# Performance work log

Measured on AMD Instinct MI355X. Metric: run time of the kernel, lower is better.

The kernel has to match this reference:

```python
import jax, jax.numpy as jnp
import numpy as np

B, L, D, H, DFF = 8, 1024, 256, 8, 2048
DH = D // H


def setup_inputs() -> dict:
    key = jax.random.key(0)
    ks = jax.random.split(key, 12)

    def w(k, shape):
        return jax.random.normal(k, shape, dtype=jnp.float32) * 0.02

    # continuous padding: first `length` tokens valid, rest padded (mask True = pad)
    lengths = jax.random.randint(ks[0], (B,), L // 4, L + 1)
    mask = jnp.arange(L)[None, :] >= lengths[:, None]

    return {
        "src": jax.random.normal(ks[1], (B, L, D), dtype=jnp.float32),
        "src_key_padding_mask": mask,
        "in_proj_w": w(ks[2], (3 * D, D)),
        "in_proj_b": w(ks[3], (3 * D,)),
        "out_w": w(ks[4], (D, D)),
        "out_b": w(ks[5], (D,)),
        "proj_w": w(ks[6], (D, D)),
        "proj_b": w(ks[7], (D,)),
        "ff1_w": w(ks[8], (DFF, D)),
        "ff1_b": w(ks[9], (DFF,)),
        "ff2_w": w(ks[10], (D, DFF)),
        "ff2_b": w(ks[11], (D,)),
    }


def reference(src, src_key_padding_mask, in_proj_w, in_proj_b, out_w, out_b,
              proj_w, proj_b, ff1_w, ff1_b, ff2_w, ff2_b):
    mask = src_key_padding_mask  # [B, L], True = padding
    neg_inf = jnp.float32(-jnp.inf)

    # --- make_attn_mask (vectorized, continuous padding) ---
    s = (~mask).sum(axis=1).astype(jnp.float32)              # [B] valid lengths
    idx = jnp.arange(L, dtype=jnp.float32)
    dist = jnp.abs(idx[:, None] - idx[None, :])              # [L, L]
    valid_tok = idx[None, :] < s[:, None]                    # [B, L]
    pair_ok = valid_tok[:, :, None] & valid_tok[:, None, :]  # [B, L, L]
    bias = jnp.where(pair_ok, (s[:, None, None] - dist[None]) / s[:, None, None], neg_inf)
    # rows that are entirely -inf (padded query rows) are zeroed, like masked_fill
    row_pad = ~valid_tok                                     # [B, L]
    bias = jnp.where(row_pad[:, :, None], 0.0, bias)
    # key_padding_mask is merged additively (as in nn.MultiheadAttention)
    add_mask = bias + jnp.where(mask[:, None, :], neg_inf, 0.0)  # [B, L, L]

    # --- multi-head self-attention ---
    qkv = src @ in_proj_w.T + in_proj_b                      # [B, L, 3D]
    q, k, v = jnp.split(qkv, 3, axis=-1)

    def heads(t):
        return t.reshape(B, L, H, DH).transpose(0, 2, 1, 3)  # [B, H, L, DH]

    q, k, v = heads(q), heads(k), heads(v)
    scale = 1.0 / jnp.sqrt(jnp.float32(DH))
    scores = jnp.einsum('bhqd,bhkd->bhqk', q, k) * scale + add_mask[:, None]
    attn = jax.nn.softmax(scores, axis=-1)
    ctx = jnp.einsum('bhqk,bhkd->bhqd', attn, v)
    ctx = ctx.transpose(0, 2, 1, 3).reshape(B, L, D)
    h_attn = ctx @ out_w.T + out_b

    # --- residual proj + FFN (no layernorm, no dropout) ---
    h = src + (h_attn @ proj_w.T + proj_b)
    ff = jax.nn.gelu(h @ ff1_w.T + ff1_b, approximate=False) @ ff2_w.T + ff2_b
    h = h + ff

    # zero out padded rows (masked_fill with all_neg_inf)
    h = jnp.where(row_pad[:, :, None], 0.0, h)
    return h
```

## Files before the change

### kernel.cpp

```cpp
#include <hip/hip_runtime.h>
#include <hip/hip_bf16.h>


#define BB   8
#define LL   1024
#define DD   256
#define HHN  8
#define DHH  32
#define DFFN 2048

typedef __attribute__((ext_vector_type(8))) __bf16 bf16x8;
typedef __attribute__((ext_vector_type(4))) float f32x4;

__device__ inline void gload16(const void* g, void* l) {
  __builtin_amdgcn_global_load_lds(
      (const __attribute__((address_space(1))) void*)g,
      (__attribute__((address_space(3))) void*)l, 16, 0, 0);
}

__device__ inline bf16x8 cvt8(const float4 a, const float4 b) {
  bf16x8 o;
  o[0] = (__bf16)a.x; o[1] = (__bf16)a.y; o[2] = (__bf16)a.z; o[3] = (__bf16)a.w;
  o[4] = (__bf16)b.x; o[5] = (__bf16)b.y; o[6] = (__bf16)b.z; o[7] = (__bf16)b.w;
  return o;
}

#define NCVT2 (DFFN * DD)
#define NCVT3 (DD * DFFN)
#define NB_CVT ((NCVT2 + NCVT3) / 2048)

__global__ __launch_bounds__(256) void preamble_kernel(
    const unsigned char* __restrict__ mb, const float* __restrict__ ff1_w,
    const float* __restrict__ ff2_w, const float* __restrict__ proj_w,
    const float* __restrict__ out_w, const float* __restrict__ proj_b,
    const float* __restrict__ out_b, __hip_bfloat16* __restrict__ wff1_bf,
    __hip_bfloat16* __restrict__ wff2_bf, __hip_bfloat16* __restrict__ wc_bf,
    float* __restrict__ bc, int* __restrict__ lens) {
  const int bid = blockIdx.x;
  const int tid = threadIdx.x;
  __shared__ float red[256];
  __shared__ int cnt[BB];
  __shared__ int flag3f, flagNA;

  if (bid < NB_CVT) {
    int i = bid * 2048 + tid * 8;
    const float* s;
    __hip_bfloat16* d;
    if (i < NCVT2) { s = ff1_w; d = wff1_bf; }
    else { s = ff2_w; d = wff2_bf; i -= NCVT2; }
    const float4 a = *(const float4*)(s + i);
    const float4 b = *(const float4*)(s + i + 4);
    *(bf16x8*)(d + i) = cvt8(a, b);
  } else if (bid == NB_CVT) {
    if (tid == 0) { flag3f = 0; flagNA = 0; }
    if (tid < BB) cnt[tid] = 0;
    __syncthreads();
    for (int i = tid; i < BB * LL; i += 256) {
      unsigned char v = mb[i];
      if (v) {
        if ((i & 3) == 3 && v == 0x3F) flag3f = 1;
        else if (i & 3) flagNA = 1;
      }
    }
    __syncthreads();
    const bool isfloat = (flag3f != 0);
    const bool isbool = (!isfloat) && (flagNA != 0);
    if (isbool) {
      for (int i = tid; i < BB * LL; i += 256)
        if (mb[i] == 0) atomicAdd(&cnt[i >> 10], 1);
    } else {
      const int* mi = (const int*)mb;
      for (int i = tid; i < BB * LL; i += 256)
        if (mi[i] == 0) atomicAdd(&cnt[i >> 10], 1);
    }
    __syncthreads();
    if (tid < BB) lens[tid] = cnt[tid];
  } else {
    const int i0 = (bid - NB_CVT - 1) << 2;
    const int k = tid;
    float acc[4] = {0.f, 0.f, 0.f, 0.f};
    for (int n = 0; n < DD; ++n) {
      const float won = out_w[n * DD + k];
#pragma unroll
      for (int j = 0; j < 4; ++j)
        acc[j] = fmaf(proj_w[(i0 + j) * DD + n], won, acc[j]);
    }
#pragma unroll
    for (int j = 0; j < 4; ++j) wc_bf[(i0 + j) * DD + k] = (__hip_bfloat16)acc[j];
#pragma unroll
    for (int j = 0; j < 4; ++j) {
      red[k] = proj_w[(i0 + j) * DD + k] * out_b[k];
      __syncthreads();
      for (int sft = 128; sft > 0; sft >>= 1) {
        if (k < sft) red[k] += red[k + sft];
        __syncthreads();
      }
      if (k == 0) bc[i0 + j] = proj_b[i0 + j] + red[0];
      __syncthreads();
    }
  }
}

__global__ __launch_bounds__(256) void gemm_qkv(
    const float* __restrict__ A, const float* __restrict__ W,
    const float* __restrict__ bias, __hip_bfloat16* __restrict__ Cb,
    const int* __restrict__ lens) {
  __shared__ __bf16 As[2][128][32];
  __shared__ __bf16 Bs[2][128][32];

  const int tid = threadIdx.x;
  const int w = tid >> 6;
  const int lane = tid & 63;
  const int c = lane & 15;
  const int hq = lane >> 4;
  const int h8 = hq << 3;
  const int wr = w >> 1, wc = w & 1;
  const int c0 = blockIdx.x << 7;
  const int r0 = blockIdx.y << 7;
  if ((r0 & (LL - 1)) >= lens[r0 >> 10]) return;

  const int srow = tid >> 2;
  const int scol = (tid & 3) << 3;

  float4 ra[2][2], rb[2][2];
  auto LOADR = [&](int kt) {
    const int k0 = kt << 5;
#pragma unroll
    for (int ch = 0; ch < 2; ++ch) {
      const float* ap = A + (size_t)(r0 + (ch << 6) + srow) * DD + k0 + scol;
      ra[ch][0] = *(const float4*)ap;
      ra[ch][1] = *(const float4*)(ap + 4);
      const float* wp = W + (size_t)(c0 + (ch << 6) + srow) * DD + k0 + scol;
      rb[ch][0] = *(const float4*)wp;
      rb[ch][1] = *(const float4*)(wp + 4);
    }
  };
  auto WRITEL = [&](int buf) {
#pragma unroll
    for (int ch = 0; ch < 2; ++ch) {
      *(bf16x8*)&As[buf][(ch << 6) + srow][scol] = cvt8(ra[ch][0], ra[ch][1]);
      *(bf16x8*)&Bs[buf][(ch << 6) + srow][scol] = cvt8(rb[ch][0], rb[ch][1]);
    }
  };

  f32x4 acc[4][4];
#pragma unroll
  for (int m = 0; m < 4; ++m)
#pragma unroll
    for (int n = 0; n < 4; ++n) acc[m][n] = (f32x4){0.f, 0.f, 0.f, 0.f};

  int buf = 0;
  LOADR(0);
  WRITEL(0);
  __syncthreads();
  for (int kt = 0; kt < 8; ++kt) {
    if (kt + 1 < 8) LOADR(kt + 1);
    bf16x8 af[4], bfr[4];
#pragma unroll
    for (int m = 0; m < 4; ++m)
      af[m] = *(const bf16x8*)&As[buf][wr * 64 + (m << 4) + c][h8];
#pragma unroll
    for (int n = 0; n < 4; ++n)
      bfr[n] = *(const bf16x8*)&Bs[buf][(wc << 6) + (n << 4) + c][h8];
#pragma unroll
    for (int m = 0; m < 4; ++m)
#pragma unroll
      for (int n = 0; n < 4; ++n)
        acc[m][n] =
            __builtin_amdgcn_mfma_f32_16x16x32_bf16(af[m], bfr[n], acc[m][n], 0, 0, 0);
    if (kt + 1 < 8) WRITEL(buf ^ 1);
    __syncthreads();
    buf ^= 1;
  }

  float bv[4];
#pragma unroll
  for (int n = 0; n < 4; ++n) bv[n] = bias[c0 + (wc << 6) + (n << 4) + c];
#pragma unroll
  for (int m = 0; m < 4; ++m)
#pragma unroll
    for (int i = 0; i < 4; ++i) {
      const int gr = r0 + wr * 64 + (m << 4) + (hq << 2) + i;
#pragma unroll
      for (int n = 0; n < 4; ++n)
        Cb[(size_t)gr * 768 + c0 + (wc << 6) + (n << 4) + c] =
            (__hip_bfloat16)(acc[m][n][i] + bv[n]);
    }
}

template <int EPI, int BM>
__global__ __launch_bounds__(256) void gemm_bf16(
    const __hip_bfloat16* __restrict__ A, const __hip_bfloat16* __restrict__ W,
    const float* __restrict__ bias, const float* __restrict__ resid,
    float* __restrict__ Cf, __hip_bfloat16* __restrict__ Cb, const int M,
    const int N, const int K, const int* __restrict__ lens) {
  constexpr int MF = BM / 32;
  constexpr int CH = BM / 64;
  __shared__ __bf16 As[2][BM][32];
  __shared__ __bf16 Bs[2][128][32];

  const int tid = threadIdx.x;
  const int w = tid >> 6;
  const int lane = tid & 63;
  const int c = lane & 15;
  const int hq = lane >> 4;
  const int h8 = hq << 3;
  const int wr = w >> 1, wc = w & 1;
  const int c0 = blockIdx.x << 7;
  const int r0 = blockIdx.y * BM;
  if ((r0 & (LL - 1)) >= lens[r0 >> 10]) return;

  const int srow = tid >> 2;
  const int scol = (tid & 3) << 3;

  auto STAGE = [&](int buf, int kt) {
    const int k0 = kt << 5;
#pragma unroll
    for (int ch = 0; ch < CH; ++ch)
      gload16(A + (size_t)(r0 + (ch << 6) + srow) * K + k0 + scol,
              &As[buf][(ch << 6) + (w << 4)][0]);
#pragma unroll
    for (int ch = 0; ch < 2; ++ch)
      gload16(W + (size_t)(c0 + (ch << 6) + srow) * K + k0 + scol,
              &Bs[buf][(ch << 6) + (w << 4)][0]);
  };

  f32x4 acc[MF][4];
#pragma unroll
  for (int m = 0; m < MF; ++m)
#pragma unroll
    for (int n = 0; n < 4; ++n) acc[m][n] = (f32x4){0.f, 0.f, 0.f, 0.f};

  const int nkt = K >> 5;
  int buf = 0;
  STAGE(0, 0);
  __syncthreads();
  for (int kt = 0; kt < nkt; ++kt) {
    if (kt + 1 < nkt) STAGE(buf ^ 1, kt + 1);
    bf16x8 af[MF], bfr[4];
#pragma unroll
    for (int m = 0; m < MF; ++m)
      af[m] = *(const bf16x8*)&As[buf][wr * (MF * 16) + (m << 4) + c][h8];
#pragma unroll
    for (int n = 0; n < 4; ++n)
      bfr[n] = *(const bf16x8*)&Bs[buf][(wc << 6) + (n << 4) + c][h8];
#pragma unroll
    for (int m = 0; m < MF; ++m)
#pragma unroll
      for (int n = 0; n < 4; ++n)
        acc[m][n] =
            __builtin_amdgcn_mfma_f32_16x16x32_bf16(af[m], bfr[n], acc[m][n], 0, 0, 0);
    __syncthreads();
    buf ^= 1;
  }

  float bv[4];
#pragma unroll
  for (int n = 0; n < 4; ++n) bv[n] = bias[c0 + (wc << 6) + (n << 4) + c];

#pragma unroll
  for (int m = 0; m < MF; ++m) {
#pragma unroll
    for (int i = 0; i < 4; ++i) {
      const int gr = r0 + wr * (MF * 16) + (m << 4) + (hq << 2) + i;
#pragma unroll
      for (int n = 0; n < 4; ++n) {
        const int gc = c0 + (wc << 6) + (n << 4) + c;
        float v = acc[m][n][i] + bv[n];
        if (EPI == 1) v = 0.5f * v * (1.0f + erff(v * 0.70710678118654752f));
        if (EPI == 2) {
          v += resid[(size_t)gr * N + gc];
          Cf[(size_t)gr * N + gc] = v;
        }
        Cb[(size_t)gr * N + gc] = (__hip_bfloat16)v;
      }
    }
  }
}

__global__ __launch_bounds__(256) void gemm_ff2_part(
    const __hip_bfloat16* __restrict__ A, const __hip_bfloat16* __restrict__ W,
    __hip_bfloat16* __restrict__ P, const int* __restrict__ lens) {
  constexpr int MF = 2;
  __shared__ __bf16 As[2][64][32];
  __shared__ __bf16 Bs[2][128][32];

  const int tid = threadIdx.x;
  const int w = tid >> 6;
  const int lane = tid & 63;
  const int c = lane & 15;
  const int hq = lane >> 4;
  const int h8 = hq << 3;
  const int wr = w >> 1, wc = w & 1;
  const int c0 = blockIdx.x << 7;
  const int r0 = blockIdx.y << 6;
  if ((r0 & (LL - 1)) >= lens[r0 >> 10]) return;

  const int kz = blockIdx.z;
  const int kbase = kz << 9;
  const int srow = tid >> 2;
  const int scol = (tid & 3) << 3;

  auto STAGE = [&](int buf, int kt) {
    const int k0 = kbase + (kt << 5);
    gload16(A + (size_t)(r0 + srow) * DFFN + k0 + scol, &As[buf][w << 4][0]);
#pragma unroll
    for (int ch = 0; ch < 2; ++ch)
      gload16(W + (size_t)(c0 + (ch << 6) + srow) * DFFN + k0 + scol,
              &Bs[buf][(ch << 6) + (w << 4)][0]);
  };

  f32x4 acc[MF][4];
#pragma unroll
  for (int m = 0; m < MF; ++m)
#pragma unroll
    for (int n = 0; n < 4; ++n) acc[m][n] = (f32x4){0.f, 0.f, 0.f, 0.f};

  int buf = 0;
  STAGE(0, 0);
  __syncthreads();
  for (int kt = 0; kt < 16; ++kt) {
    if (kt + 1 < 16) STAGE(buf ^ 1, kt + 1);
    bf16x8 af[MF], bfr[4];
#pragma unroll
    for (int m = 0; m < MF; ++m)
      af[m] = *(const bf16x8*)&As[buf][wr * (MF * 16) + (m << 4) + c][h8];
#pragma unroll
    for (int n = 0; n < 4; ++n)
      bfr[n] = *(const bf16x8*)&Bs[buf][(wc << 6) + (n << 4) + c][h8];
#pragma unroll
    for (int m = 0; m < MF; ++m)
#pragma unroll
      for (int n = 0; n < 4; ++n)
        acc[m][n] =
            __builtin_amdgcn_mfma_f32_16x16x32_bf16(af[m], bfr[n], acc[m][n], 0, 0, 0);
    __syncthreads();
    buf ^= 1;
  }

  __hip_bfloat16* Pz = P + (size_t)kz * (BB * LL) * DD;
#pragma unroll
  for (int m = 0; m < MF; ++m)
#pragma unroll
    for (int i = 0; i < 4; ++i) {
      const int gr = r0 + wr * (MF * 16) + (m << 4) + (hq << 2) + i;
#pragma unroll
      for (int n = 0; n < 4; ++n)
        Pz[(size_t)gr * DD + c0 + (wc << 6) + (n << 4) + c] =
            (__hip_bfloat16)acc[m][n][i];
    }
}

__global__ __launch_bounds__(256) void ff2_reduce(
    const __hip_bfloat16* __restrict__ P, const float* __restrict__ resid,
    const float* __restrict__ bias, float* __restrict__ out,
    const int* __restrict__ lens) {
  const int idx = blockIdx.x * 256 + threadIdx.x;
  const int r = idx >> 6;
  const int c4 = (idx & 63) << 2;
  float4 o;
  if ((r & (LL - 1)) >= lens[r >> 10]) {
    o.x = o.y = o.z = o.w = 0.f;
  } else {
    const size_t base = (size_t)r * DD + c4;
    o = *(const float4*)&resid[base];
    const float4 bv = *(const float4*)&bias[c4];
    o.x += bv.x; o.y += bv.y; o.z += bv.z; o.w += bv.w;
#pragma unroll
    for (int z = 0; z < 4; ++z) {
      const __hip_bfloat16* pz = P + (size_t)z * (BB * LL) * DD + base;
      ushort4 pu = *(const ushort4*)pz;
      o.x += __bfloat162float(*(const __hip_bfloat16*)&pu.x);
      o.y += __bfloat162float(*(const __hip_bfloat16*)&pu.y);
      o.z += __bfloat162float(*(const __hip_bfloat16*)&pu.z);
      o.w += __bfloat162float(*(const __hip_bfloat16*)&pu.w);
    }
  }
  *(float4*)&out[(size_t)r * DD + c4] = o;
}

__global__ __launch_bounds__(256) void attn_fwd_mfma(
    const __hip_bfloat16* __restrict__ qkv, __hip_bfloat16* __restrict__ ctx,
    const int* __restrict__ lens) {
  __shared__ __bf16 Ks[2][64][56];
  __shared__ __bf16 Vt[2][32][66];
  __shared__ __bf16 Pl[4][16][72];

  const int tid = threadIdx.x;
  const int q0 = blockIdx.x << 6;
  const int hh = blockIdx.y;
  const int b = blockIdx.z;
  const int slen = lens[b];
  if (q0 >= slen) return;

  const int w = tid >> 6;
  const int lane = tid & 63;
  const int c = lane & 15;
  const int h = lane >> 4;
  const int h8 = h << 3;

  const float L2E = 1.44269504f;
  const float sf = (float)slen;
  const float cb = -7.0f * L2E;
  const float cd = (1.0f / sf) * L2E;
  const float qscale = 0.17677669529663689f * L2E;

  bf16x8 qf;
  {
    const int qrow = q0 + (w << 4) + c;
    const bf16x8 qraw =
        *(const bf16x8*)(qkv + (size_t)(b * LL + qrow) * 768 + hh * DHH + h8);
#pragma unroll
    for (int j = 0; j < 8; ++j) qf[j] = (__bf16)((float)qraw[j] * qscale);
  }

  f32x4 acc0 = {0.f, 0.f, 0.f, 0.f};
  f32x4 acc1 = {0.f, 0.f, 0.f, 0.f};
  float lsum[4] = {0.f, 0.f, 0.f, 0.f};

  const int skey = tid >> 2;
  const int sdg = (tid & 3) << 3;
  const int ntk = (slen + 63) >> 6;
  const int qg = q0 + (w << 4) + (h << 2);

  const __hip_bfloat16* kvbase = qkv + (size_t)b * LL * 768 + 256 + hh * DHH + sdg;

  bf16x8 kreg, vreg;
  {
    const __hip_bfloat16* kb = kvbase + (size_t)skey * 768;
    kreg = *(const bf16x8*)kb;
    vreg = *(const bf16x8*)(kb + 256);
    *(bf16x8*)&Ks[0][skey][sdg] = kreg;
#pragma unroll
    for (int j = 0; j < 8; ++j) Vt[0][sdg + j][skey] = vreg[j];
  }
  if (ntk > 1) {
    const __hip_bfloat16* kb = kvbase + (size_t)(64 + skey) * 768;
    kreg = *(const bf16x8*)kb;
    vreg = *(const bf16x8*)(kb + 256);
  }
  __syncthreads();

  for (int kt = 0; kt < ntk; ++kt) {
    const int p = kt & 1;
    const int kbase = kt << 6;

    f32x4 st[4];
    __builtin_amdgcn_s_setprio(1);
#pragma unroll
    for (int t = 0; t < 4; ++t) {
      const bf16x8 kf = *(const bf16x8*)&Ks[p][(t << 4) + c][h8];
      st[t] = __builtin_amdgcn_mfma_f32_16x16x32_bf16(
          qf, kf, (f32x4){0.f, 0.f, 0.f, 0.f}, 0, 0, 0);
    }
    __builtin_amdgcn_s_setprio(0);

    if (kbase + 64 <= slen) {
#pragma unroll
      for (int t = 0; t < 4; ++t) {
        const float kjf = (float)(kbase + (t << 4) + c);
#pragma unroll
        for (int i = 0; i < 4; ++i) {
          const float dist = fabsf((float)(qg + i) - kjf);
          const float pv = __builtin_amdgcn_exp2f(st[t][i] + cb - dist * cd);
          lsum[i] += pv;
          Pl[w][(h << 2) + i][c + (t << 4)] = (__bf16)pv;
        }
      }
    } else {
#pragma unroll
      for (int t = 0; t < 4; ++t) {
        const int kj = kbase + (t << 4) + c;
        const bool kvalid = kj < slen;
        const float kjf = (float)kj;
#pragma unroll
        for (int i = 0; i < 4; ++i) {
          const float dist = fabsf((float)(qg + i) - kjf);
          const float arg = kvalid ? (st[t][i] + cb - dist * cd) : -1e30f;
          const float pv = __builtin_amdgcn_exp2f(arg);
          lsum[i] += pv;
          Pl[w][(h << 2) + i][c + (t << 4)] = (__bf16)pv;
        }
      }
    }

    asm volatile("s_waitcnt lgkmcnt(0)" ::: "memory");

    __builtin_amdgcn_s_setprio(1);
#pragma unroll
    for (int n = 0; n < 2; ++n) {
      const bf16x8 pf = *(const bf16x8*)&Pl[w][c][h8 + (n << 5)];
      const uint32_t* v0p = (const uint32_t*)&Vt[p][c][h8 + (n << 5)];
      const uint32_t* v1p = (const uint32_t*)&Vt[p][16 + c][h8 + (n << 5)];
      union { uint32_t u[4]; bf16x8 v; } t0, t1;
#pragma unroll
      for (int j = 0; j < 4; ++j) { t0.u[j] = v0p[j]; t1.u[j] = v1p[j]; }
      acc0 = __builtin_amdgcn_mfma_f32_16x16x32_bf16(pf, t0.v, acc0, 0, 0, 0);
      acc1 = __builtin_amdgcn_mfma_f32_16x16x32_bf16(pf, t1.v, acc1, 0, 0, 0);
    }
    __builtin_amdgcn_s_setprio(0);

    if (kt + 1 < ntk) {
      *(bf16x8*)&Ks[p ^ 1][skey][sdg] = kreg;
#pragma unroll
      for (int j = 0; j < 8; ++j) Vt[p ^ 1][sdg + j][skey] = vreg[j];
      if (kt + 2 < ntk) {
        const __hip_bfloat16* kb = kvbase + (size_t)(((kt + 2) << 6) + skey) * 768;
        kreg = *(const bf16x8*)kb;
        vreg = *(const bf16x8*)(kb + 256);
      }
    }
    __syncthreads();
  }

#pragma unroll
  for (int i = 0; i < 4; ++i) {
    float l = lsum[i];
    l += __shfl_xor(l, 1);
    l += __shfl_xor(l, 2);
    l += __shfl_xor(l, 4);
    l += __shfl_xor(l, 8);
    const float il = 1.0f / l;
    __hip_bfloat16* op =
        ctx + (size_t)(b * LL + q0 + (w << 4) + (h << 2) + i) * 256 + hh * DHH;
    op[c] = (__hip_bfloat16)(acc0[i] * il);
    op[c + 16] = (__hip_bfloat16)(acc1[i] * il);
  }
}

extern "C" void kernel_launch(void* const* d_in, const int* in_sizes, int n_in,
                              void* d_out, int out_size, void* d_ws,
                              size_t ws_size, hipStream_t stream) {
  (void)in_sizes; (void)n_in; (void)out_size; (void)ws_size;
  const float* src = (const float*)d_in[0];
  const unsigned char* mask = (const unsigned char*)d_in[1];
  const float* in_proj_w = (const float*)d_in[2];
  const float* in_proj_b = (const float*)d_in[3];
  const float* out_w = (const float*)d_in[4];
  const float* out_b = (const float*)d_in[5];
  const float* proj_w = (const float*)d_in[6];
  const float* proj_b = (const float*)d_in[7];
  const float* ff1_w = (const float*)d_in[8];
  const float* ff1_b = (const float*)d_in[9];
  const float* ff2_w = (const float*)d_in[10];
  const float* ff2_b = (const float*)d_in[11];
  float* out = (float*)d_out;

  const int M = BB * LL;
  char* p = (char*)d_ws;
  __hip_bfloat16* qkv_bf = (__hip_bfloat16*)p; p += (size_t)M * 768 * 2;
  __hip_bfloat16* ctx_bf = (__hip_bfloat16*)p; p += (size_t)M * 256 * 2;
  float* hbuf_f = (float*)p;                    p += (size_t)M * 256 * 4;
  __hip_bfloat16* hbuf_bf = (__hip_bfloat16*)p; p += (size_t)M * 256 * 2;
  __hip_bfloat16* ff1o_bf = (__hip_bfloat16*)p; p += (size_t)M * 2048 * 2;
  __hip_bfloat16* wff1_bf = (__hip_bfloat16*)p; p += (size_t)2048 * 256 * 2;
  __hip_bfloat16* wff2_bf = (__hip_bfloat16*)p; p += (size_t)256 * 2048 * 2;
  __hip_bfloat16* wc_bf = (__hip_bfloat16*)p;   p += (size_t)256 * 256 * 2;
  float* bc = (float*)p;                        p += 256 * 4;
  int* lens = (int*)p;                          p += 256;
  __hip_bfloat16* pbuf = (__hip_bfloat16*)p;    p += (size_t)4 * M * 256 * 2;

  preamble_kernel<<<NB_CVT + 1 + 64, 256, 0, stream>>>(
      mask, ff1_w, ff2_w, proj_w, out_w, proj_b, out_b, wff1_bf, wff2_bf,
      wc_bf, bc, lens);

  gemm_qkv<<<dim3(6, 64), 256, 0, stream>>>(src, in_proj_w, in_proj_b, qkv_bf,
                                            lens);
  attn_fwd_mfma<<<dim3(LL / 64, HHN, BB), 256, 0, stream>>>(qkv_bf, ctx_bf, lens);
  gemm_bf16<2, 64><<<dim3(2, 128), 256, 0, stream>>>(
      ctx_bf, wc_bf, bc, src, hbuf_f, hbuf_bf, M, 256, 256, lens);
  gemm_bf16<1, 128><<<dim3(16, 64), 256, 0, stream>>>(
      hbuf_bf, wff1_bf, ff1_b, nullptr, nullptr, ff1o_bf, M, 2048, 256, lens);
  gemm_ff2_part<<<dim3(2, 128, 4), 256, 0, stream>>>(ff1o_bf, wff2_bf, pbuf, lens);
  ff2_reduce<<<M * 256 / 4 / 256, 256, 0, stream>>>(pbuf, hbuf_f, ff2_b, out, lens);
}
```

Measured before the change: 126.3 us.

## Fuse preamble with QKV GEMM and fold split-K FF2 reduction into last block

The QKV projection now runs with 64-row tiles inside the same launch as the weight conversion, length counting and combined-weight blocks, removing one kernel launch. Because lengths are computed in that same launch, the QKV GEMM can no longer skip padded rows. The separate FF2 reduction kernel is removed: each split-K block bumps a per-tile atomic counter, and the last arriving block sums the partials with the residual and bias. Fully padded tiles write zeros directly. The output-projection GEMM is retiled to 64x64 to launch more blocks. The trade-off is fewer launches and better parallelism against extra QKV work on padding rows and the cost of atomics and fences.

```diff
diff --git a/kernel.cpp b/kernel.cpp
--- a/kernel.cpp
+++ b/kernel.cpp
@@ -27,23 +27,110 @@
 
 #define NCVT2 (DFFN * DD)
 #define NCVT3 (DD * DFFN)
-#define NB_CVT ((NCVT2 + NCVT3) / 2048)
-
-__global__ __launch_bounds__(256) void preamble_kernel(
-    const unsigned char* __restrict__ mb, const float* __restrict__ ff1_w,
-    const float* __restrict__ ff2_w, const float* __restrict__ proj_w,
-    const float* __restrict__ out_w, const float* __restrict__ proj_b,
-    const float* __restrict__ out_b, __hip_bfloat16* __restrict__ wff1_bf,
+#define NB_QKV 768
+#define NB_CVT 512
+#define BID_LENS (NB_QKV + NB_CVT)
+#define NB_TOTAL (BID_LENS + 1 + 64)
+
+__global__ __launch_bounds__(256) void fused_pre_qkv(
+    const float* __restrict__ src, const unsigned char* __restrict__ mb,
+    const float* __restrict__ in_proj_w, const float* __restrict__ in_proj_b,
+    const float* __restrict__ ff1_w, const float* __restrict__ ff2_w,
+    const float* __restrict__ proj_w, const float* __restrict__ out_w,
+    const float* __restrict__ proj_b, const float* __restrict__ out_b,
+    __hip_bfloat16* __restrict__ qkv_bf, __hip_bfloat16* __restrict__ wff1_bf,
     __hip_bfloat16* __restrict__ wff2_bf, __hip_bfloat16* __restrict__ wc_bf,
-    float* __restrict__ bc, int* __restrict__ lens) {
+    float* __restrict__ bc, int* __restrict__ lens, int* __restrict__ cnt) {
+  __shared__ __bf16 As[2][64][32];
+  __shared__ __bf16 Bs[2][128][32];
+  __shared__ float red[256];
+  __shared__ int cnt8[BB];
+  __shared__ int flag3f, flagNA;
+
   const int bid = blockIdx.x;
   const int tid = threadIdx.x;
-  __shared__ float red[256];
-  __shared__ int cnt[BB];
-  __shared__ int flag3f, flagNA;
-
-  if (bid < NB_CVT) {
-    int i = bid * 2048 + tid * 8;
+
+  if (bid < NB_QKV) {
+    const int x = bid % 6;
+    const int y = bid / 6;
+    const int c0 = x << 7;
+    const int r0 = y << 6;
+    const int w = tid >> 6;
+    const int lane = tid & 63;
+    const int c = lane & 15;
+    const int hq = lane >> 4;
+    const int h8 = hq << 3;
+    const int wr = w >> 1, wc2 = w & 1;
+    const int srow = tid >> 2;
+    const int scol = (tid & 3) << 3;
+
+    float4 ra[2], rb[2][2];
+    auto LOADR = [&](int kt) {
+      const int k0 = kt << 5;
+      const float* ap = src + (size_t)(r0 + srow) * DD + k0 + scol;
+      ra[0] = *(const float4*)ap;
+      ra[1] = *(const float4*)(ap + 4);
+#pragma unroll
+      for (int ch = 0; ch < 2; ++ch) {
+        const float* wp =
+            in_proj_w + (size_t)(c0 + (ch << 6) + srow) * DD + k0 + scol;
+        rb[ch][0] = *(const float4*)wp;
+        rb[ch][1] = *(const float4*)(wp + 4);
+      }
+    };
+    auto WRITEL = [&](int buf) {
+      *(bf16x8*)&As[buf][srow][scol] = cvt8(ra[0], ra[1]);
+#pragma unroll
+      for (int ch = 0; ch < 2; ++ch)
+        *(bf16x8*)&Bs[buf][(ch << 6) + srow][scol] = cvt8(rb[ch][0], rb[ch][1]);
+    };
+
+    f32x4 acc[2][4];
+#pragma unroll
+    for (int m = 0; m < 2; ++m)
+#pragma unroll
+      for (int n = 0; n < 4; ++n) acc[m][n] = (f32x4){0.f, 0.f, 0.f, 0.f};
+
+    int buf = 0;
+    LOADR(0);
+    WRITEL(0);
+    __syncthreads();
+    for (int kt = 0; kt < 8; ++kt) {
+      if (kt + 1 < 8) LOADR(kt + 1);
+      bf16x8 af[2], bfr[4];
+#pragma unroll
+      for (int m = 0; m < 2; ++m)
+        af[m] = *(const bf16x8*)&As[buf][wr * 32 + (m << 4) + c][h8];
+#pragma unroll
+      for (int n = 0; n < 4; ++n)
+        bfr[n] = *(const bf16x8*)&Bs[buf][(wc2 << 6) + (n << 4) + c][h8];
+#pragma unroll
+      for (int m = 0; m < 2; ++m)
+#pragma unroll
+        for (int n = 0; n < 4; ++n)
+          acc[m][n] = __builtin_amdgcn_mfma_f32_16x16x32_bf16(af[m], bfr[n],
+                                                              acc[m][n], 0, 0, 0);
+      if (kt + 1 < 8) WRITEL(buf ^ 1);
+      __syncthreads();
+      buf ^= 1;
+    }
+
+    float bv[4];
+#pragma unroll
+    for (int n = 0; n < 4; ++n)
+      bv[n] = in_proj_b[c0 + (wc2 << 6) + (n << 4) + c];
+#pragma unroll
+    for (int m = 0; m < 2; ++m)
+#pragma unroll
+      for (int i = 0; i < 4; ++i) {
+        const int gr = r0 + wr * 32 + (m << 4) + (hq << 2) + i;
+#pragma unroll
+        for (int n = 0; n < 4; ++n)
+          qkv_bf[(size_t)gr * 768 + c0 + (wc2 << 6) + (n << 4) + c] =
+              (__hip_bfloat16)(acc[m][n][i] + bv[n]);
+      }
+  } else if (bid < BID_LENS) {
+    int i = (bid - NB_QKV) * 2048 + tid * 8;
     const float* s;
     __hip_bfloat16* d;
     if (i < NCVT2) { s = ff1_w; d = wff1_bf; }
@@ -51,9 +138,10 @@
     const float4 a = *(const float4*)(s + i);
     const float4 b = *(const float4*)(s + i + 4);
     *(bf16x8*)(d + i) = cvt8(a, b);
-  } else if (bid == NB_CVT) {
+  } else if (bid == BID_LENS) {
+    cnt[tid] = 0;
     if (tid == 0) { flag3f = 0; flagNA = 0; }
-    if (tid < BB) cnt[tid] = 0;
+    if (tid < BB) cnt8[tid] = 0;
     __syncthreads();
     for (int i = tid; i < BB * LL; i += 256) {
       unsigned char v = mb[i];
@@ -67,16 +155,16 @@
     const bool isbool = (!isfloat) && (flagNA != 0);
     if (isbool) {
       for (int i = tid; i < BB * LL; i += 256)
-        if (mb[i] == 0) atomicAdd(&cnt[i >> 10], 1);
+        if (mb[i] == 0) atomicAdd(&cnt8[i >> 10], 1);
     } else {
       const int* mi = (const int*)mb;
       for (int i = tid; i < BB * LL; i += 256)
-        if (mi[i] == 0) atomicAdd(&cnt[i >> 10], 1);
+        if (mi[i] == 0) atomicAdd(&cnt8[i >> 10], 1);
     }
     __syncthreads();
-    if (tid < BB) lens[tid] = cnt[tid];
+    if (tid < BB) lens[tid] = cnt8[tid];
   } else {
-    const int i0 = (bid - NB_CVT - 1) << 2;
+    const int i0 = (bid - BID_LENS - 1) << 2;
     const int k = tid;
     float acc[4] = {0.f, 0.f, 0.f, 0.f};
     for (int n = 0; n < DD; ++n) {
@@ -101,12 +189,18 @@
   }
 }
 
-__global__ __launch_bounds__(256) void gemm_qkv(
-    const float* __restrict__ A, const float* __restrict__ W,
-    const float* __restrict__ bias, __hip_bfloat16* __restrict__ Cb,
-    const int* __restrict__ lens) {
-  __shared__ __bf16 As[2][128][32];
-  __shared__ __bf16 Bs[2][128][32];
+template <int EPI, int BM, int BN>
+__global__ __launch_bounds__(256) void gemm_bf16(
+    const __hip_bfloat16* __restrict__ A, const __hip_bfloat16* __restrict__ W,
+    const float* __restrict__ bias, const float* __restrict__ resid,
+    float* __restrict__ Cf, __hip_bfloat16* __restrict__ Cb, const int M,
+    const int N, const int K, const int* __restrict__ lens) {
+  constexpr int MF = BM / 32;
+  constexpr int NF = BN / 32;
+  constexpr int CHA = BM / 64;
+  constexpr int CHB = BN / 64;
+  __shared__ __bf16 As[2][BM][32];
+  __shared__ __bf16 Bs[2][BN][32];
 
   const int tid = threadIdx.x;
   const int w = tid >> 6;
@@ -115,121 +209,30 @@
   const int hq = lane >> 4;
   const int h8 = hq << 3;
   const int wr = w >> 1, wc = w & 1;
-  const int c0 = blockIdx.x << 7;
-  const int r0 = blockIdx.y << 7;
+  const int c0 = blockIdx.x * BN;
+  const int r0 = blockIdx.y * BM;
   if ((r0 & (LL - 1)) >= lens[r0 >> 10]) return;
 
   const int srow = tid >> 2;
   const int scol = (tid & 3) << 3;
 
-  float4 ra[2][2], rb[2][2];
-  auto LOADR = [&](int kt) {
-    const int k0 = kt << 5;
-#pragma unroll
-    for (int ch = 0; ch < 2; ++ch) {
-      const float* ap = A + (size_t)(r0 + (ch << 6) + srow) * DD + k0 + scol;
-      ra[ch][0] = *(const float4*)ap;
-      ra[ch][1] = *(const float4*)(ap + 4);
-      const float* wp = W + (size_t)(c0 + (ch << 6) + srow) * DD + k0 + scol;
-      rb[ch][0] = *(const float4*)wp;
-      rb[ch][1] = *(const float4*)(wp + 4);
-    }
-  };
-  auto WRITEL = [&](int buf) {
-#pragma unroll
-    for (int ch = 0; ch < 2; ++ch) {
-      *(bf16x8*)&As[buf][(ch << 6) + srow][scol] = cvt8(ra[ch][0], ra[ch][1]);
-      *(bf16x8*)&Bs[buf][(ch << 6) + srow][scol] = cvt8(rb[ch][0], rb[ch][1]);
-    }
-  };
-
-  f32x4 acc[4][4];
-#pragma unroll
-  for (int m = 0; m < 4; ++m)
-#pragma unroll
-    for (int n = 0; n < 4; ++n) acc[m][n] = (f32x4){0.f, 0.f, 0.f, 0.f};
-
-  int buf = 0;
-  LOADR(0);
-  WRITEL(0);
-  __syncthreads();
-  for (int kt = 0; kt < 8; ++kt) {
-    if (kt + 1 < 8) LOADR(kt + 1);
-    bf16x8 af[4], bfr[4];
-#pragma unroll
-    for (int m = 0; m < 4; ++m)
-      af[m] = *(const bf16x8*)&As[buf][wr * 64 + (m << 4) + c][h8];
-#pragma unroll
-    for (int n = 0; n < 4; ++n)
-      bfr[n] = *(const bf16x8*)&Bs[buf][(wc << 6) + (n << 4) + c][h8];
-#pragma unroll
-    for (int m = 0; m < 4; ++m)
-#pragma unroll
-      for (int n = 0; n < 4; ++n)
-        acc[m][n] =
-            __builtin_amdgcn_mfma_f32_16x16x32_bf16(af[m], bfr[n], acc[m][n], 0, 0, 0);
-    if (kt + 1 < 8) WRITEL(buf ^ 1);
-    __syncthreads();
-    buf ^= 1;
-  }
-
-  float bv[4];
-#pragma unroll
-  for (int n = 0; n < 4; ++n) bv[n] = bias[c0 + (wc << 6) + (n << 4) + c];
-#pragma unroll
-  for (int m = 0; m < 4; ++m)
-#pragma unroll
-    for (int i = 0; i < 4; ++i) {
-      const int gr = r0 + wr * 64 + (m << 4) + (hq << 2) + i;
-#pragma unroll
-      for (int n = 0; n < 4; ++n)
-        Cb[(size_t)gr * 768 + c0 + (wc << 6) + (n << 4) + c] =
-            (__hip_bfloat16)(acc[m][n][i] + bv[n]);
-    }
-}
-
-template <int EPI, int BM>
-__global__ __launch_bounds__(256) void gemm_bf16(
-    const __hip_bfloat16* __restrict__ A, const __hip_bfloat16* __restrict__ W,
-    const float* __restrict__ bias, const float* __restrict__ resid,
-    float* __restrict__ Cf, __hip_bfloat16* __restrict__ Cb, const int M,
-    const int N, const int K, const int* __restrict__ lens) {
-  constexpr int MF = BM / 32;
-  constexpr int CH = BM / 64;
-  __shared__ __bf16 As[2][BM][32];
-  __shared__ __bf16 Bs[2][128][32];
-
-  const int tid = threadIdx.x;
-  const int w = tid >> 6;
-  const int lane = tid & 63;
-  const int c = lane & 15;
-  const int hq = lane >> 4;
-  const int h8 = hq << 3;
-  const int wr = w >> 1, wc = w & 1;
-  const int c0 = blockIdx.x << 7;
-  const int r0 = blockIdx.y * BM;
-  if ((r0 & (LL - 1)) >= lens[r0 >> 10]) return;
-
-  const int srow = tid >> 2;
-  const int scol = (tid & 3) << 3;
-
   auto STAGE = [&](int buf, int kt) {
     const int k0 = kt << 5;
 #pragma unroll
-    for (int ch = 0; ch < CH; ++ch)
+    for (int ch = 0; ch < CHA; ++ch)
       gload16(A + (size_t)(r0 + (ch << 6) + srow) * K + k0 + scol,
               &As[buf][(ch << 6) + (w << 4)][0]);
 #pragma unroll
-    for (int ch = 0; ch < 2; ++ch)
+    for (int ch = 0; ch < CHB; ++ch)
       gload16(W + (size_t)(c0 + (ch << 6) + srow) * K + k0 + scol,
               &Bs[buf][(ch << 6) + (w << 4)][0]);
   };
 
-  f32x4 acc[MF][4];
+  f32x4 acc[MF][NF];
 #pragma unroll
   for (int m = 0; m < MF; ++m)
 #pragma unroll
-    for (int n = 0; n < 4; ++n) acc[m][n] = (f32x4){0.f, 0.f, 0.f, 0.f};
+    for (int n = 0; n < NF; ++n) acc[m][n] = (f32x4){0.f, 0.f, 0.f, 0.f};
 
   const int nkt = K >> 5;
   int buf = 0;
@@ -237,26 +240,26 @@
   __syncthreads();
   for (int kt = 0; kt < nkt; ++kt) {
     if (kt + 1 < nkt) STAGE(buf ^ 1, kt + 1);
-    bf16x8 af[MF], bfr[4];
+    bf16x8 af[MF], bfr[NF];
 #pragma unroll
     for (int m = 0; m < MF; ++m)
       af[m] = *(const bf16x8*)&As[buf][wr * (MF * 16) + (m << 4) + c][h8];
 #pragma unroll
-    for (int n = 0; n < 4; ++n)
-      bfr[n] = *(const bf16x8*)&Bs[buf][(wc << 6) + (n << 4) + c][h8];
+    for (int n = 0; n < NF; ++n)
+      bfr[n] = *(const bf16x8*)&Bs[buf][wc * (NF * 16) + (n << 4) + c][h8];
 #pragma unroll
     for (int m = 0; m < MF; ++m)
 #pragma unroll
-      for (int n = 0; n < 4; ++n)
+      for (int n = 0; n < NF; ++n)
         acc[m][n] =
             __builtin_amdgcn_mfma_f32_16x16x32_bf16(af[m], bfr[n], acc[m][n], 0, 0, 0);
     __syncthreads();
     buf ^= 1;
   }
 
-  float bv[4];
-#pragma unroll
-  for (int n = 0; n < 4; ++n) bv[n] = bias[c0 + (wc << 6) + (n << 4) + c];
+  float bv[NF];
+#pragma unroll
+  for (int n = 0; n < NF; ++n) bv[n] = bias[c0 + wc * (NF * 16) + (n << 4) + c];
 
 #pragma unroll
   for (int m = 0; m < MF; ++m) {
@@ -264,8 +267,8 @@
     for (int i = 0; i < 4; ++i) {
       const int gr = r0 + wr * (MF * 16) + (m << 4) + (hq << 2) + i;
 #pragma unroll
-      for (int n = 0; n < 4; ++n) {
-        const int gc = c0 + (wc << 6) + (n << 4) + c;
+      for (int n = 0; n < NF; ++n) {
+        const int gc = c0 + wc * (NF * 16) + (n << 4) + c;
         float v = acc[m][n][i] + bv[n];
         if (EPI == 1) v = 0.5f * v * (1.0f + erff(v * 0.70710678118654752f));
         if (EPI == 2) {
@@ -278,12 +281,14 @@
   }
 }
 
-__global__ __launch_bounds__(256) void gemm_ff2_part(
+__global__ __launch_bounds__(256) void gemm_ff2_fused(
     const __hip_bfloat16* __restrict__ A, const __hip_bfloat16* __restrict__ W,
-    __hip_bfloat16* __restrict__ P, const int* __restrict__ lens) {
-  constexpr int MF = 2;
+    const float* __restrict__ resid, const float* __restrict__ bias,
+    float* __restrict__ out, __hip_bfloat16* __restrict__ P,
+    int* __restrict__ cnt, const int* __restrict__ lens) {
   __shared__ __bf16 As[2][64][32];
   __shared__ __bf16 Bs[2][128][32];
+  __shared__ int is_red;
 
   const int tid = threadIdx.x;
   const int w = tid >> 6;
@@ -294,7 +299,22 @@
   const int wr = w >> 1, wc = w & 1;
   const int c0 = blockIdx.x << 7;
   const int r0 = blockIdx.y << 6;
-  if ((r0 & (LL - 1)) >= lens[r0 >> 10]) return;
+  const int tile = (blockIdx.y << 1) | blockIdx.x;
+  const int mylen = lens[r0 >> 10];
+
+  if ((r0 & (LL - 1)) >= mylen) {
+    if (blockIdx.z == 0) {
+#pragma unroll
+      for (int k = 0; k < 8; ++k) {
+        const int f4 = k * 256 + tid;
+        const int rr = f4 >> 5;
+        const int cc = (f4 & 31) << 2;
+        *(float4*)&out[(size_t)(r0 + rr) * DD + c0 + cc] =
+            (float4){0.f, 0.f, 0.f, 0.f};
+      }
+    }
+    return;
+  }
 
   const int kz = blockIdx.z;
   const int kbase = kz << 9;
@@ -310,9 +330,9 @@
               &Bs[buf][(ch << 6) + (w << 4)][0]);
   };
 
-  f32x4 acc[MF][4];
-#pragma unroll
-  for (int m = 0; m < MF; ++m)
+  f32x4 acc[2][4];
+#pragma unroll
+  for (int m = 0; m < 2; ++m)
 #pragma unroll
     for (int n = 0; n < 4; ++n) acc[m][n] = (f32x4){0.f, 0.f, 0.f, 0.f};
 
@@ -321,15 +341,15 @@
   __syncthreads();
   for (int kt = 0; kt < 16; ++kt) {
     if (kt + 1 < 16) STAGE(buf ^ 1, kt + 1);
-    bf16x8 af[MF], bfr[4];
-#pragma unroll
-    for (int m = 0; m < MF; ++m)
-      af[m] = *(const bf16x8*)&As[buf][wr * (MF * 16) + (m << 4) + c][h8];
+    bf16x8 af[2], bfr[4];
+#pragma unroll
+    for (int m = 0; m < 2; ++m)
+      af[m] = *(const bf16x8*)&As[buf][wr * 32 + (m << 4) + c][h8];
 #pragma unroll
     for (int n = 0; n < 4; ++n)
       bfr[n] = *(const bf16x8*)&Bs[buf][(wc << 6) + (n << 4) + c][h8];
 #pragma unroll
-    for (int m = 0; m < MF; ++m)
+    for (int m = 0; m < 2; ++m)
 #pragma unroll
       for (int n = 0; n < 4; ++n)
         acc[m][n] =
@@ -340,43 +360,50 @@
 
   __hip_bfloat16* Pz = P + (size_t)kz * (BB * LL) * DD;
 #pragma unroll
-  for (int m = 0; m < MF; ++m)
+  for (int m = 0; m < 2; ++m)
 #pragma unroll
     for (int i = 0; i < 4; ++i) {
-      const int gr = r0 + wr * (MF * 16) + (m << 4) + (hq << 2) + i;
+      const int gr = r0 + wr * 32 + (m << 4) + (hq << 2) + i;
 #pragma unroll
       for (int n = 0; n < 4; ++n)
         Pz[(size_t)gr * DD + c0 + (wc << 6) + (n << 4) + c] =
             (__hip_bfloat16)acc[m][n][i];
     }
-}
-
-__global__ __launch_bounds__(256) void ff2_reduce(
-    const __hip_bfloat16* __restrict__ P, const float* __restrict__ resid,
-    const float* __restrict__ bias, float* __restrict__ out,
-    const int* __restrict__ lens) {
-  const int idx = blockIdx.x * 256 + threadIdx.x;
-  const int r = idx >> 6;
-  const int c4 = (idx & 63) << 2;
-  float4 o;
-  if ((r & (LL - 1)) >= lens[r >> 10]) {
-    o.x = o.y = o.z = o.w = 0.f;
-  } else {
-    const size_t base = (size_t)r * DD + c4;
-    o = *(const float4*)&resid[base];
-    const float4 bv = *(const float4*)&bias[c4];
-    o.x += bv.x; o.y += bv.y; o.z += bv.z; o.w += bv.w;
-#pragma unroll
-    for (int z = 0; z < 4; ++z) {
-      const __hip_bfloat16* pz = P + (size_t)z * (BB * LL) * DD + base;
-      ushort4 pu = *(const ushort4*)pz;
-      o.x += __bfloat162float(*(const __hip_bfloat16*)&pu.x);
-      o.y += __bfloat162float(*(const __hip_bfloat16*)&pu.y);
-      o.z += __bfloat162float(*(const __hip_bfloat16*)&pu.z);
-      o.w += __bfloat162float(*(const __hip_bfloat16*)&pu.w);
-    }
-  }
-  *(float4*)&out[(size_t)r * DD + c4] = o;
+
+  __threadfence();
+  __syncthreads();
+  if (tid == 0) is_red = (atomicAdd(&cnt[tile], 1) == 3);
+  __syncthreads();
+  if (!is_red) return;
+  __threadfence();
+
+#pragma unroll
+  for (int k = 0; k < 8; ++k) {
+    const int f4 = k * 256 + tid;
+    const int rr = f4 >> 5;
+    const int cc = (f4 & 31) << 2;
+    const int grow = r0 + rr;
+    float4 o;
+    if ((grow & (LL - 1)) >= mylen) {
+      o.x = o.y = o.z = o.w = 0.f;
+    } else {
+      const size_t base = (size_t)grow * DD + c0 + cc;
+      o = *(const float4*)&resid[base];
+      const float4 bvv = *(const float4*)&bias[c0 + cc];
+      o.x += bvv.x; o.y += bvv.y; o.z += bvv.z; o.w += bvv.w;
+#pragma unroll
+      for (int z = 0; z < 4; ++z) {
+        const ushort4 pu =
+            *(const ushort4*)(P + (size_t)z * (BB * LL) * DD + base);
+        o.x += __bfloat162float(*(const __hip_bfloat16*)&pu.x);
+        o.y += __bfloat162float(*(const __hip_bfloat16*)&pu.y);
+        o.z += __bfloat162float(*(const __hip_bfloat16*)&pu.z);
+        o.w += __bfloat162float(*(const __hip_bfloat16*)&pu.w);
+      }
+    }
+    *(float4*)&out[(size_t)grow * DD + c0 + cc] = o;
+  }
+  if (tid == 0) cnt[tile] = 0;
 }
 
 __global__ __launch_bounds__(256) void attn_fwd_mfma(
@@ -558,19 +585,21 @@
   __hip_bfloat16* wc_bf = (__hip_bfloat16*)p;   p += (size_t)256 * 256 * 2;
   float* bc = (float*)p;                        p += 256 * 4;
   int* lens = (int*)p;                          p += 256;
+  int* cnt = (int*)p;                           p += 1024;
   __hip_bfloat16* pbuf = (__hip_bfloat16*)p;    p += (size_t)4 * M * 256 * 2;
 
-  preamble_kernel<<<NB_CVT + 1 + 64, 256, 0, stream>>>(
-      mask, ff1_w, ff2_w, proj_w, out_w, proj_b, out_b, wff1_bf, wff2_bf,
-      wc_bf, bc, lens);
-
-  gemm_qkv<<<dim3(6, 64), 256, 0, stream>>>(src, in_proj_w, in_proj_b, qkv_bf,
-                                            lens);
+  fused_pre_qkv<<<NB_TOTAL, 256, 0, stream>>>(
+      src, mask, in_proj_w, in_proj_b, ff1_w, ff2_w, proj_w, out_w, proj_b,
+      out_b, qkv_bf, wff1_bf, wff2_bf, wc_bf, bc, lens, cnt);
+
   attn_fwd_mfma<<<dim3(LL / 64, HHN, BB), 256, 0, stream>>>(qkv_bf, ctx_bf, lens);
-  gemm_bf16<2, 64><<<dim3(2, 128), 256, 0, stream>>>(
+
+  gemm_bf16<2, 64, 64><<<dim3(4, 128), 256, 0, stream>>>(
       ctx_bf, wc_bf, bc, src, hbuf_f, hbuf_bf, M, 256, 256, lens);
-  gemm_bf16<1, 128><<<dim3(16, 64), 256, 0, stream>>>(
+
+  gemm_bf16<1, 128, 128><<<dim3(16, 64), 256, 0, stream>>>(
       hbuf_bf, wff1_bf, ff1_b, nullptr, nullptr, ff1o_bf, M, 2048, 256, lens);
-  gemm_ff2_part<<<dim3(2, 128, 4), 256, 0, stream>>>(ff1o_bf, wff2_bf, pbuf, lens);
-  ff2_reduce<<<M * 256 / 4 / 256, 256, 0, stream>>>(pbuf, hbuf_f, ff2_b, out, lens);
+
+  gemm_ff2_fused<<<dim3(2, 128, 4), 256, 0, stream>>>(
+      ff1o_bf, wff2_bf, hbuf_f, ff2_b, out, pbuf, cnt, lens);
 }
```

Result: slower. 248.5 us (+96.8%).
